# Optimization experiments

Hardware: AMD Instinct MI355X
Metric: run time of the kernel (lower is better)

## Reference

```python
import jax, jax.numpy as jnp
import numpy as np

B, T, D, H, L, F = 256, 32, 1024, 8, 3, 2048
SSRC, NCOL, NTAB, NACT, NSYM = 64, 32, 16, 64, 32
HD = D // H


def setup_inputs() -> dict:
    key = jax.random.key(0)
    ks = jax.random.split(key, 40)
    n = lambda k, s, sc=0.02: jax.random.normal(k, s, jnp.float32) * sc
    inp = {}
    inp["prev_action_emb"] = jax.random.normal(ks[0], (B, T, D), jnp.float32)
    inp["encoded_src"] = jax.random.normal(ks[1], (B, SSRC, D), jnp.float32)
    inp["encoded_col"] = jax.random.normal(ks[2], (B, NCOL, D), jnp.float32)
    inp["encoded_tab"] = jax.random.normal(ks[3], (B, NTAB, D), jnp.float32)
    inp["src_mask"] = jnp.zeros((B, SSRC), jnp.int32)  # 1 = padded
    inp["symbol_ids"] = jax.random.randint(ks[4], (B, T), 0, NSYM)
    inp["view_type"] = jax.random.randint(ks[5], (B,), 0, 3)  # 0=action,1=col,2=tab
    inp["gold_action"] = jax.random.randint(ks[6], (B,), 0, NACT)
    inp["gold_col"] = jax.random.randint(ks[7], (B,), 0, NCOL)
    inp["gold_tab"] = jax.random.randint(ks[8], (B,), 0, NTAB)
    # grammar embeddings (torch nn.Embedding default ~ N(0,1))
    inp["symbol_emb"] = jax.random.normal(ks[9], (NSYM, D), jnp.float32)
    inp["action_emb"] = jax.random.normal(ks[10], (NACT, D), jnp.float32)
    # affine heads
    inp["action_aff_w"] = n(ks[11], (D, D)); inp["action_aff_b"] = jnp.zeros((D,), jnp.float32)
    inp["symbol_aff_w"] = n(ks[12], (D, D)); inp["symbol_aff_b"] = jnp.zeros((D,), jnp.float32)
    inp["col_aff_w"] = n(ks[13], (D, D)); inp["col_aff_b"] = jnp.zeros((D,), jnp.float32)
    inp["tab_aff_w"] = n(ks[14], (D, D)); inp["tab_aff_b"] = jnp.zeros((D,), jnp.float32)
    inp["tgt_lin_w"] = n(ks[15], (2 * D, D)); inp["tgt_lin_b"] = jnp.zeros((D,), jnp.float32)
    inp["out_lin_w"] = n(ks[16], (D, D)); inp["out_lin_b"] = jnp.zeros((D,), jnp.float32)
    # transformer decoder layers (q,k,v,o stacked on axis 1)
    inp["self_w"] = n(ks[17], (L, 4, D, D)); inp["self_b"] = jnp.zeros((L, 4, D), jnp.float32)
    inp["cross_w"] = n(ks[18], (L, 4, D, D)); inp["cross_b"] = jnp.zeros((L, 4, D), jnp.float32)
    inp["ffn_w1"] = n(ks[19], (L, D, F)); inp["ffn_b1"] = jnp.zeros((L, F), jnp.float32)
    inp["ffn_w2"] = n(ks[20], (L, F, D)); inp["ffn_b2"] = jnp.zeros((L, D), jnp.float32)
    inp["ln_g"] = jnp.ones((L, 3, D), jnp.float32); inp["ln_b"] = jnp.zeros((L, 3, D), jnp.float32)
    return inp


def _pe(t, d):
    pos = jnp.arange(t, dtype=jnp.float32)[:, None]
    div = jnp.exp(jnp.arange(0, d, 2, dtype=jnp.float32) * (-np.log(10000.0) / d))
    pe = jnp.zeros((t, d), jnp.float32)
    pe = pe.at[:, 0::2].set(jnp.sin(pos * div)).at[:, 1::2].set(jnp.cos(pos * div))
    return pe


def _ln(x, g, b, eps=1e-5):
    m = jnp.mean(x, -1, keepdims=True)
    v = jnp.mean((x - m) ** 2, -1, keepdims=True)
    return (x - m) / jnp.sqrt(v + eps) * g + b


def _mha(xq, xkv, w, b, pad=None):
    # w: [4, D, D] for q,k,v,o; pad: [B, Tk] bool key-padding mask
    q = (xq @ w[0] + b[0]).reshape(xq.shape[0], -1, H, HD)
    k = (xkv @ w[1] + b[1]).reshape(xkv.shape[0], -1, H, HD)
    v = (xkv @ w[2] + b[2]).reshape(xkv.shape[0], -1, H, HD)
    s = jnp.einsum("bqhd,bkhd->bhqk", q, k) / np.sqrt(HD).astype(np.float32)
    if pad is not None:
        s = jnp.where(pad[:, None, None, :], -1e9, s)
    a = jax.nn.softmax(s, -1)
    o = jnp.einsum("bhqk,bkhd->bqhd", a, v).reshape(xq.shape[0], -1, D)
    return o @ w[3] + b[3]


def reference(prev_action_emb, encoded_src, encoded_col, encoded_tab, symbol_emb, action_emb,
              action_aff_w, action_aff_b, symbol_aff_w, symbol_aff_b, col_aff_w, col_aff_b,
              tab_aff_w, tab_aff_b, tgt_lin_w, tgt_lin_b, out_lin_w, out_lin_b,
              self_w, self_b, cross_w, cross_b, ffn_w1, ffn_b1, ffn_w2, ffn_b2, ln_g, ln_b,
              src_mask, symbol_ids, view_type, gold_action, gold_col, gold_tab):
    # target embeddings: affine(prev action emb) ++ affine(symbol emb gather)
    tgt_a = prev_action_emb @ action_aff_w + action_aff_b            # [B,T,D]
    tgt_s = symbol_emb[symbol_ids] @ symbol_aff_w + symbol_aff_b     # [B,T,D]
    x = jnp.concatenate([tgt_a, tgt_s], -1) @ tgt_lin_w + tgt_lin_b  # [B,T,D]
    x = x + _pe(T, D)[None]  # positional encoding (dropout = eval identity)
    pad = src_mask.astype(bool)
    for l in range(L):  # post-LN TransformerDecoderLayer (torch default, relu FFN)
        x = _ln(x + _mha(x, x, self_w[l], self_b[l]), ln_g[l, 0], ln_b[l, 0])
        x = _ln(x + _mha(x, encoded_src, cross_w[l], cross_b[l], pad), ln_g[l, 1], ln_b[l, 1])
        ff = jax.nn.relu(x @ ffn_w1[l] + ffn_b1[l]) @ ffn_w2[l] + ffn_b2[l]
        x = _ln(x + ff, ln_g[l, 2], ln_b[l, 2])
    out = x[:, -1, :] @ out_lin_w + out_lin_b  # [B,D], last decode position
    # three routed prediction heads: affine(src) . out -> masked log_softmax
    src_a = action_emb @ action_aff_w + action_aff_b                 # [A,D]
    logp_a = jax.nn.log_softmax(out @ src_a.T, -1)                   # [B,A]
    src_c = encoded_col @ col_aff_w + col_aff_b                      # [B,Nc,D]
    logp_c = jax.nn.log_softmax(jnp.einsum("bnd,bd->bn", src_c, out), -1)
    src_t = encoded_tab @ tab_aff_w + tab_aff_b                      # [B,Nt,D]
    logp_t = jax.nn.log_softmax(jnp.einsum("bnd,bd->bn", src_t, out), -1)
    ga = jnp.take_along_axis(logp_a, gold_action[:, None], 1)[:, 0]
    gc = jnp.take_along_axis(logp_c, gold_col[:, None], 1)[:, 0]
    gt = jnp.take_along_axis(logp_t, gold_tab[:, None], 1)[:, 0]
    # grammar routing: each example's loss comes from exactly one view
    nll = -jnp.where(view_type == 0, ga, jnp.where(view_type == 1, gc, gt))  # [B]
    return nll
```

## Files before the change

### kernel.cpp

```cpp
#include <hip/hip_runtime.h>

typedef float  f32x4 __attribute__((ext_vector_type(4)));
typedef short  s16x8 __attribute__((ext_vector_type(8)));

__device__ __forceinline__ float b2f(short s) {
    return __uint_as_float(((unsigned)(unsigned short)s) << 16);
}
__device__ __forceinline__ short f2b(float f) {
    unsigned u = __float_as_uint(f);
    u = u + 0x7fffu + ((u >> 16) & 1u);
    return (short)(u >> 16);
}

__device__ __forceinline__ void gld_lds16(const short* g, short* l) {
    __builtin_amdgcn_global_load_lds(
        (const __attribute__((address_space(1))) unsigned int*)(const void*)g,
        (__attribute__((address_space(3))) unsigned int*)(void*)l,
        16, 0, 0);
}

#define S_VMCNT0    asm volatile("s_waitcnt vmcnt(0)" ::: "memory")
#define S_LGKM0     asm volatile("s_waitcnt lgkmcnt(0)" ::: "memory")
#define SBAR        __builtin_amdgcn_s_barrier()
#define SCHED0      __builtin_amdgcn_sched_barrier(0)

template<int BM>
__global__ __launch_bounds__(512) void gemm_pipe(
    const short* __restrict__ A, const short* __restrict__ Bt,
    const float* __restrict__ bias,
    short* __restrict__ Cb,
    const short* __restrict__ res,
    const float* __restrict__ sym2, const int* __restrict__ sid,
    const float* __restrict__ pe,
    int M, int N, int K, int epi)
{
    constexpr int MF   = BM / 32;
    constexpr int ALW  = BM / 64;
    constexpr int BUFB = (BM + 256) * 128;
    __shared__ short lds[2 * (BM + 256) * 64];

    const int tid  = threadIdx.x;
    const int lane = tid & 63;
    const int wave = tid >> 6;

    int bid = blockIdx.x;
    int nwg = gridDim.x;
    if ((nwg & 7) == 0) { int q = nwg >> 3; bid = (bid & 7) * q + (bid >> 3); }
    const int nbx = N >> 8;
    const int m0 = (bid / nbx) * BM;
    const int n0 = (bid % nbx) * 256;

    const int wm = (wave >> 2) * (BM / 2);
    const int wn = (wave & 3) * 64;
    const int l15 = lane & 15, l4 = lane >> 4;
    const int key = lane & 7;

    f32x4 acc[MF][4];
#pragma unroll
    for (int m = 0; m < MF; m++)
#pragma unroll
        for (int n = 0; n < 4; n++)
#pragma unroll
            for (int j = 0; j < 4; j++) acc[m][n][j] = 0.f;

    int aoff[MF], boff[4];
#pragma unroll
    for (int m = 0; m < MF; m++) {
        int r = wm + m * 16 + l15;
        aoff[m] = r * 128 + ((l4 ^ key) << 4);
    }
#pragma unroll
    for (int n = 0; n < 4; n++) {
        int r = wn + n * 16 + l15;
        boff[n] = BM * 128 + r * 128 + ((l4 ^ key) << 4);
    }

    const int lrow = lane >> 3;
    const int lchunk = (lane & 7) ^ lrow;
    size_t agoff[ALW]; int aldo[ALW];
#pragma unroll
    for (int i = 0; i < ALW; i++) {
        int rr = wave * (BM / 8) + i * 8;
        agoff[i] = (size_t)(m0 + rr + lrow) * K + lchunk * 8;
        aldo[i]  = rr * 128;
    }
    size_t bgoff[4]; int bldo[4];
#pragma unroll
    for (int i = 0; i < 4; i++) {
        int rr = wave * 32 + i * 8;
        bgoff[i] = (size_t)(n0 + rr + lrow) * K + lchunk * 8;
        bldo[i]  = BM * 128 + rr * 128;
    }

    char* lbase = (char*)lds;
    auto stage = [&](int kt, int bufoff) {
        char* lb = lbase + bufoff;
        const size_t ke = (size_t)kt * 64;
#pragma unroll
        for (int i = 0; i < ALW; i++)
            gld_lds16(A + agoff[i] + ke, (short*)(lb + aldo[i]));
#pragma unroll
        for (int i = 0; i < 4; i++)
            gld_lds16(Bt + bgoff[i] + ke, (short*)(lb + bldo[i]));
    };

    const int NT = K >> 6;
    stage(0, 0);
    S_VMCNT0; SCHED0; SBAR; SCHED0;

    int cb = 0;
    for (int t = 0; t < NT; t++) {
        if (t + 1 < NT) stage(t + 1, (cb ^ 1) * BUFB);
        const char* cp = lbase + cb * BUFB;
        {
            s16x8 af[MF], bv[4];
#pragma unroll
            for (int m = 0; m < MF; m++) af[m] = *(const s16x8*)(cp + aoff[m]);
#pragma unroll
            for (int n = 0; n < 4; n++)  bv[n] = *(const s16x8*)(cp + boff[n]);
            S_LGKM0; SCHED0;
            __builtin_amdgcn_s_setprio(1);
#pragma unroll
            for (int m = 0; m < MF; m++)
#pragma unroll
                for (int n = 0; n < 4; n++)
                    acc[m][n] = __builtin_amdgcn_mfma_f32_16x16x32_bf16(
                        af[m], bv[n], acc[m][n], 0, 0, 0);
            __builtin_amdgcn_s_setprio(0);
        }
        {
            s16x8 af[MF], bv[4];
#pragma unroll
            for (int m = 0; m < MF; m++) af[m] = *(const s16x8*)(cp + (aoff[m] ^ 64));
#pragma unroll
            for (int n = 0; n < 4; n++)  bv[n] = *(const s16x8*)(cp + (boff[n] ^ 64));
            S_LGKM0; SCHED0;
            __builtin_amdgcn_s_setprio(1);
#pragma unroll
            for (int m = 0; m < MF; m++)
#pragma unroll
                for (int n = 0; n < 4; n++)
                    acc[m][n] = __builtin_amdgcn_mfma_f32_16x16x32_bf16(
                        af[m], bv[n], acc[m][n], 0, 0, 0);
            __builtin_amdgcn_s_setprio(0);
        }
        S_VMCNT0; SCHED0; SBAR; SCHED0;
        cb ^= 1;
    }

#pragma unroll
    for (int m = 0; m < MF; m++) {
#pragma unroll
        for (int n = 0; n < 4; n++) {
#pragma unroll
            for (int j = 0; j < 4; j++) {
                int row = m0 + wm + m * 16 + l4 * 4 + j;
                int col = n0 + wn + n * 16 + l15;
                float v = acc[m][n][j];
                if (bias) v += bias[col];
                size_t idx = (size_t)row * N + col;
                if (epi == 0) {
                    Cb[idx] = f2b(v);
                } else if (epi == 2) {
                    v += sym2[(size_t)sid[row] * 1024 + col] + pe[(size_t)(row & 31) * 1024 + col];
                    Cb[idx] = f2b(v);
                } else if (epi == 3) {
                    Cb[idx] = f2b(fmaxf(v, 0.f));
                } else {
                    Cb[idx] = f2b(v + b2f(res[idx]));
                }
            }
        }
    }
}

__global__ __launch_bounds__(256) void gemm_bt(
    const short* __restrict__ A, const short* __restrict__ Bt,
    const float* __restrict__ bias,
    float* __restrict__ Cf, short* __restrict__ Cb,
    const short* __restrict__ res,
    int M, int N, int K, int epi)
{
    __shared__ short As[128 * 64];
    __shared__ short Bs[128 * 64];
    const int tid  = threadIdx.x;
    const int lane = tid & 63;
    const int wave = tid >> 6;
    const int m0 = blockIdx.y * 128, n0 = blockIdx.x * 128;
    const int wm = (wave >> 1) * 64, wn = (wave & 1) * 64;
    const int l15 = lane & 15, l4 = lane >> 4;

    f32x4 acc[4][4];
#pragma unroll
    for (int m = 0; m < 4; m++)
#pragma unroll
        for (int n = 0; n < 4; n++)
#pragma unroll
            for (int j = 0; j < 4; j++) acc[m][n][j] = 0.f;

    const int srow = wave * 32 + (lane >> 3);
    const int scol = (lane & 7) * 8;
    const short* Ag = A  + (size_t)(m0 + srow) * K + scol;
    const short* Bg = Bt + (size_t)(n0 + srow) * K + scol;
    short* Al = As + (wave * 32) * 64;
    short* Bl = Bs + (wave * 32) * 64;

    for (int k0 = 0; k0 < K; k0 += 64) {
#pragma unroll
        for (int i = 0; i < 4; i++) {
            gld_lds16(Ag + (size_t)(i * 8) * K + k0, Al + i * 8 * 64);
            gld_lds16(Bg + (size_t)(i * 8) * K + k0, Bl + i * 8 * 64);
        }
        __syncthreads();
#pragma unroll
        for (int kk = 0; kk < 64; kk += 32) {
            s16x8 af[4], bfv[4];
#pragma unroll
            for (int m = 0; m < 4; m++)
                af[m] = *(const s16x8*)(As + (wm + m * 16 + l15) * 64 + kk + l4 * 8);
#pragma unroll
            for (int n = 0; n < 4; n++)
                bfv[n] = *(const s16x8*)(Bs + (wn + n * 16 + l15) * 64 + kk + l4 * 8);
#pragma unroll
            for (int m = 0; m < 4; m++)
#pragma unroll
                for (int n = 0; n < 4; n++)
                    acc[m][n] = __builtin_amdgcn_mfma_f32_16x16x32_bf16(
                        af[m], bfv[n], acc[m][n], 0, 0, 0);
        }
        __syncthreads();
    }

#pragma unroll
    for (int m = 0; m < 4; m++) {
#pragma unroll
        for (int n = 0; n < 4; n++) {
#pragma unroll
            for (int j = 0; j < 4; j++) {
                int row = m0 + wm + m * 16 + l4 * 4 + j;
                int col = n0 + wn + n * 16 + l15;
                float v = acc[m][n][j];
                if (bias) v += bias[col];
                size_t idx = (size_t)row * N + col;
                if (epi == 0) {
                    Cb[idx] = f2b(v);
                } else if (epi == 1) {
                    Cf[idx] = v;
                } else if (epi == 3) {
                    Cb[idx] = f2b(fmaxf(v, 0.f));
                } else if (epi == 6) {
                    Cb[idx] = f2b(v + b2f(res[idx]));
                } else {
                    Cf[idx] = v; Cb[idx] = f2b(v);
                }
            }
        }
    }
}

__global__ __launch_bounds__(256) void attn_self(const short* __restrict__ qkv,
                                                 short* __restrict__ o)
{
    const int b = blockIdx.x >> 3, h = blockIdx.x & 7;
    __shared__ short Q[32 * 128], Kk[32 * 128], Vv[32 * 128];
    __shared__ float S[32 * 32];
    const int tid = threadIdx.x;
    const size_t base = (size_t)b * 32 * 3072 + h * 128;
    for (int i = tid; i < 512; i += 256) {
        int r = i >> 4, c = (i & 15) * 8;
        size_t g = base + (size_t)r * 3072 + c;
        *(s16x8*)(Q  + r * 128 + c) = *(const s16x8*)(qkv + g);
        *(s16x8*)(Kk + r * 128 + c) = *(const s16x8*)(qkv + g + 1024);
        *(s16x8*)(Vv + r * 128 + c) = *(const s16x8*)(qkv + g + 2048);
    }
    __syncthreads();
    for (int i = tid; i < 1024; i += 256) {
        int r = i >> 5, c = i & 31;
        float s = 0.f;
        for (int d8 = 0; d8 < 16; d8++) {
            s16x8 qa = *(const s16x8*)(Q  + r * 128 + d8 * 8);
            s16x8 ka = *(const s16x8*)(Kk + c * 128 + d8 * 8);
#pragma unroll
            for (int j = 0; j < 8; j++) s += b2f(qa[j]) * b2f(ka[j]);
        }
        S[i] = s * 0.088388347648318447f;
    }
    __syncthreads();
    if (tid < 32) {
        float mx = -1e30f;
        for (int c = 0; c < 32; c++) mx = fmaxf(mx, S[tid * 32 + c]);
        float sum = 0.f;
        for (int c = 0; c < 32; c++) { float p = __expf(S[tid * 32 + c] - mx); S[tid * 32 + c] = p; sum += p; }
        float inv = 1.f / sum;
        for (int c = 0; c < 32; c++) S[tid * 32 + c] *= inv;
    }
    __syncthreads();
    for (int i = tid; i < 4096; i += 256) {
        int r = i >> 7, d = i & 127;
        float a = 0.f;
        for (int c = 0; c < 32; c++) a += S[r * 32 + c] * b2f(Vv[c * 128 + d]);
        o[(size_t)(b * 32 + r) * 1024 + h * 128 + d] = f2b(a);
    }
}

__global__ __launch_bounds__(256) void attn_cross(const short* __restrict__ q_,
                                                  const short* __restrict__ ckv,
                                                  const int* __restrict__ mask,
                                                  short* __restrict__ o)
{
    const int b = blockIdx.x >> 3, h = blockIdx.x & 7;
    __shared__ short Q[32 * 128], Kk[64 * 128], Vv[64 * 128];
    __shared__ float S[32 * 64];
    const int tid = threadIdx.x;
    for (int i = tid; i < 512; i += 256) {
        int r = i >> 4, c = (i & 15) * 8;
        *(s16x8*)(Q + r * 128 + c) = *(const s16x8*)(q_ + (size_t)(b * 32 + r) * 1024 + h * 128 + c);
    }
    for (int i = tid; i < 1024; i += 256) {
        int r = i >> 4, c = (i & 15) * 8;
        size_t g = (size_t)(b * 64 + r) * 2048 + h * 128 + c;
        *(s16x8*)(Kk + r * 128 + c) = *(const s16x8*)(ckv + g);
        *(s16x8*)(Vv + r * 128 + c) = *(const s16x8*)(ckv + g + 1024);
    }
    __syncthreads();
    for (int i = tid; i < 2048; i += 256) {
        int r = i >> 6, c = i & 63;
        float s = 0.f;
        for (int d8 = 0; d8 < 16; d8++) {
            s16x8 qa = *(const s16x8*)(Q  + r * 128 + d8 * 8);
            s16x8 ka = *(const s16x8*)(Kk + c * 128 + d8 * 8);
#pragma unroll
            for (int j = 0; j < 8; j++) s += b2f(qa[j]) * b2f(ka[j]);
        }
        s *= 0.088388347648318447f;
        if (mask[b * 64 + c] != 0) s = -1e9f;
        S[i] = s;
    }
    __syncthreads();
    if (tid < 32) {
        float mx = -1e30f;
        for (int c = 0; c < 64; c++) mx = fmaxf(mx, S[tid * 64 + c]);
        float sum = 0.f;
        for (int c = 0; c < 64; c++) { float p = __expf(S[tid * 64 + c] - mx); S[tid * 64 + c] = p; sum += p; }
        float inv = 1.f / sum;
        for (int c = 0; c < 64; c++) S[tid * 64 + c] *= inv;
    }
    __syncthreads();
    for (int i = tid; i < 4096; i += 256) {
        int r = i >> 7, d = i & 127;
        float a = 0.f;
        for (int c = 0; c < 64; c++) a += S[r * 64 + c] * b2f(Vv[c * 128 + d]);
        o[(size_t)(b * 32 + r) * 1024 + h * 128 + d] = f2b(a);
    }
}

__global__ __launch_bounds__(256) void attn_self_last(const short* __restrict__ q,
                                                      const short* __restrict__ kv,
                                                      short* __restrict__ out)
{
    __shared__ float qs[4][128];
    __shared__ float ps[4][32];
    const int wave = threadIdx.x >> 6, lane = threadIdx.x & 63;
    const int idx = blockIdx.x * 4 + wave;
    const int b = idx >> 3, h = idx & 7;
    for (int d = lane; d < 128; d += 64)
        qs[wave][d] = b2f(q[(size_t)b * 1024 + h * 128 + d]);
    __syncthreads();
    float s = -1e30f;
    if (lane < 32) {
        const short* kr = kv + (size_t)(b * 32 + lane) * 2048 + h * 128;
        float a = 0.f;
        for (int d = 0; d < 128; d += 8) {
            s16x8 kvv = *(const s16x8*)(kr + d);
#pragma unroll
            for (int j = 0; j < 8; j++) a += qs[wave][d + j] * b2f(kvv[j]);
        }
        s = a * 0.088388347648318447f;
    }
    float mx = s;
#pragma unroll
    for (int o = 1; o < 32; o <<= 1) mx = fmaxf(mx, __shfl_xor(mx, o));
    float p = (lane < 32) ? __expf(s - mx) : 0.f;
    float sum = p;
#pragma unroll
    for (int o = 1; o < 32; o <<= 1) sum += __shfl_xor(sum, o);
    if (lane < 32) ps[wave][lane] = p / sum;
    __syncthreads();
    for (int d = lane; d < 128; d += 64) {
        float a = 0.f;
        for (int j = 0; j < 32; j++)
            a += ps[wave][j] * b2f(kv[(size_t)(b * 32 + j) * 2048 + 1024 + h * 128 + d]);
        out[(size_t)b * 1024 + h * 128 + d] = f2b(a);
    }
}

__global__ __launch_bounds__(256) void attn_cross_last(const short* __restrict__ q,
                                                       const short* __restrict__ ckv,
                                                       const int* __restrict__ mask,
                                                       short* __restrict__ out)
{
    __shared__ float qs[4][128];
    __shared__ float ps[4][64];
    const int wave = threadIdx.x >> 6, lane = threadIdx.x & 63;
    const int idx = blockIdx.x * 4 + wave;
    const int b = idx >> 3, h = idx & 7;
    for (int d = lane; d < 128; d += 64)
        qs[wave][d] = b2f(q[(size_t)b * 1024 + h * 128 + d]);
    __syncthreads();
    const short* kr = ckv + (size_t)(b * 64 + lane) * 2048 + h * 128;
    float a = 0.f;
    for (int d = 0; d < 128; d += 8) {
        s16x8 kvv = *(const s16x8*)(kr + d);
#pragma unroll
        for (int j = 0; j < 8; j++) a += qs[wave][d + j] * b2f(kvv[j]);
    }
    float s = a * 0.088388347648318447f;
    if (mask[b * 64 + lane] != 0) s = -1e9f;
    float mx = s;
#pragma unroll
    for (int o = 1; o < 64; o <<= 1) mx = fmaxf(mx, __shfl_xor(mx, o));
    float p = __expf(s - mx);
    float sum = p;
#pragma unroll
    for (int o = 1; o < 64; o <<= 1) sum += __shfl_xor(sum, o);
    ps[wave][lane] = p / sum;
    __syncthreads();
    for (int d = lane; d < 128; d += 64) {
        float acc = 0.f;
        for (int j = 0; j < 64; j++)
            acc += ps[wave][j] * b2f(ckv[(size_t)(b * 64 + j) * 2048 + 1024 + h * 128 + d]);
        out[(size_t)b * 1024 + h * 128 + d] = f2b(acc);
    }
}

__global__ __launch_bounds__(128) void ln_rows_b(const short* __restrict__ X,
                                                 short* __restrict__ Y,
                                                 const float* __restrict__ g,
                                                 const float* __restrict__ bt)
{
    const int row = blockIdx.x, tid = threadIdx.x;
    s16x8 v = *(const s16x8*)(X + (size_t)row * 1024 + tid * 8);
    float f[8];
    float s = 0.f, q = 0.f;
#pragma unroll
    for (int j = 0; j < 8; j++) { f[j] = b2f(v[j]); s += f[j]; q += f[j] * f[j]; }
#pragma unroll
    for (int o = 1; o < 64; o <<= 1) { s += __shfl_xor(s, o); q += __shfl_xor(q, o); }
    __shared__ float ls[2], lq[2];
    if ((tid & 63) == 0) { ls[tid >> 6] = s; lq[tid >> 6] = q; }
    __syncthreads();
    s = ls[0] + ls[1];
    q = lq[0] + lq[1];
    const float mean = s * 0.0009765625f;
    const float var  = q * 0.0009765625f - mean * mean;
    const float rs = rsqrtf(var + 1e-5f);
    s16x8 ov;
#pragma unroll
    for (int j = 0; j < 8; j++) {
        int c = tid * 8 + j;
        ov[j] = f2b((f[j] - mean) * rs * g[c] + bt[c]);
    }
    *(s16x8*)(Y + (size_t)row * 1024 + tid * 8) = ov;
}

__global__ __launch_bounds__(256) void convf2b(const float* __restrict__ s,
                                               short* __restrict__ d, int n)
{
    int i = (blockIdx.x * 256 + threadIdx.x) * 8;
    if (i < n) {
        float4 a = *(const float4*)(s + i);
        float4 b = *(const float4*)(s + i + 4);
        s16x8 o;
        o[0] = f2b(a.x); o[1] = f2b(a.y); o[2] = f2b(a.z); o[3] = f2b(a.w);
        o[4] = f2b(b.x); o[5] = f2b(b.y); o[6] = f2b(b.z); o[7] = f2b(b.w);
        *(s16x8*)(d + i) = o;
    }
}

__global__ __launch_bounds__(256) void transpose_conv_b(const float* __restrict__ src0,
                                                        short* __restrict__ dst0,
                                                        int R, int C)
{
    const float* src = src0 + (size_t)blockIdx.z * R * C;
    short* dst = dst0 + (size_t)blockIdx.z * R * C;
    __shared__ float t[32][33];
    int c0 = blockIdx.x * 32, r0 = blockIdx.y * 32;
    int tx = threadIdx.x & 31, ty = threadIdx.x >> 5;
#pragma unroll
    for (int i = 0; i < 32; i += 8) t[ty + i][tx] = src[(size_t)(r0 + ty + i) * C + c0 + tx];
    __syncthreads();
#pragma unroll
    for (int i = 0; i < 32; i += 8) dst[(size_t)(c0 + ty + i) * R + r0 + tx] = f2b(t[tx][ty + i]);
}

__global__ __launch_bounds__(256) void pad_conv(const float* __restrict__ s,
                                                short* __restrict__ d, int src_rows)
{
    int i = blockIdx.x * 256 + threadIdx.x;
    int r = i >> 10;
    d[i] = (r < src_rows) ? f2b(s[i]) : (short)0;
}

__global__ __launch_bounds__(256) void pe_build(float* __restrict__ pe)
{
    int i = blockIdx.x * 256 + threadIdx.x;
    int t = i >> 10, d = i & 1023;
    int de = d & ~1;
    float ang = (float)t * expf((float)de * (-9.2103403719761836f / 1024.f));
    pe[i] = (d & 1) ? cosf(ang) : sinf(ang);
}

__global__ __launch_bounds__(256) void gather_last(const short* __restrict__ x,
                                                   short* __restrict__ xlast)
{
    int i = blockIdx.x * 256 + threadIdx.x;
    int b = i >> 10, d = i & 1023;
    xlast[i] = x[((size_t)(b * 32 + 31) << 10) + d];
}

__global__ __launch_bounds__(64) void head_final(
    const float* __restrict__ logits_a,
    const float* __restrict__ enc_col_f, const short* __restrict__ yc,
    const float* __restrict__ enc_tab_f, const short* __restrict__ yt,
    const float* __restrict__ outf,
    const float* __restrict__ col_b, const float* __restrict__ tab_b,
    const int* __restrict__ view, const int* __restrict__ ga,
    const int* __restrict__ gc, const int* __restrict__ gt,
    float* __restrict__ nll)
{
    const int b = blockIdx.x, lane = threadIdx.x;
    const int vt = view[b];
    if (vt == 0) {
        float x = logits_a[(size_t)b * 128 + lane];
        float mx = x;
#pragma unroll
        for (int o = 1; o < 64; o <<= 1) mx = fmaxf(mx, __shfl_xor(mx, o));
        float sum = __expf(x - mx);
#pragma unroll
        for (int o = 1; o < 64; o <<= 1) sum += __shfl_xor(sum, o);
        float lse = mx + logf(sum);
        float gl = __shfl(x, ga[b]);
        if (lane == 0) nll[b] = lse - gl;
    } else {
        const int nit = (vt == 1) ? 32 : 16;
        const float* enc = (vt == 1) ? (enc_col_f + (size_t)b * 32 * 1024)
                                     : (enc_tab_f + (size_t)b * 16 * 1024);
        const short* y   = (vt == 1) ? (yc + (size_t)b * 1024) : (yt + (size_t)b * 1024);
        const float* bb  = (vt == 1) ? col_b : tab_b;
        float bc = 0.f;
        for (int i = lane; i < 1024; i += 64) bc += bb[i] * outf[(size_t)b * 1024 + i];
#pragma unroll
        for (int o = 1; o < 64; o <<= 1) bc += __shfl_xor(bc, o);
        float logit = -1e30f;
        if (lane < nit) {
            float s = bc;
            const float* er = enc + (size_t)lane * 1024;
            for (int d8 = 0; d8 < 128; d8++) {
                s16x8 yv = *(const s16x8*)(y + d8 * 8);
                float4 e0 = *(const float4*)(er + d8 * 8);
                float4 e1 = *(const float4*)(er + d8 * 8 + 4);
                s += e0.x * b2f(yv[0]) + e0.y * b2f(yv[1]) + e0.z * b2f(yv[2]) + e0.w * b2f(yv[3])
                   + e1.x * b2f(yv[4]) + e1.y * b2f(yv[5]) + e1.z * b2f(yv[6]) + e1.w * b2f(yv[7]);
            }
            logit = s;
        }
        float mx = logit;
#pragma unroll
        for (int o = 1; o < 64; o <<= 1) mx = fmaxf(mx, __shfl_xor(mx, o));
        float sum = (lane < nit) ? __expf(logit - mx) : 0.f;
#pragma unroll
        for (int o = 1; o < 64; o <<= 1) sum += __shfl_xor(sum, o);
        float lse = mx + logf(sum);
        int g = (vt == 1) ? gc[b] : gt[b];
        float gl = __shfl(logit, g);
        if (lane == 0) nll[b] = lse - gl;
    }
}

extern "C" void kernel_launch(void* const* d_in, const int* in_sizes, int n_in,
                              void* d_out, int out_size, void* d_ws, size_t ws_size,
                              hipStream_t stream)
{
    const float* pa_f     = (const float*)d_in[0];
    const float* src_f    = (const float*)d_in[1];
    const float* colenc_f = (const float*)d_in[2];
    const float* tabenc_f = (const float*)d_in[3];
    const int*   src_mask = (const int*)d_in[4];
    const int*   sym_ids  = (const int*)d_in[5];
    const int*   view     = (const int*)d_in[6];
    const int*   gold_a   = (const int*)d_in[7];
    const int*   gold_c   = (const int*)d_in[8];
    const int*   gold_t   = (const int*)d_in[9];
    const float* sym_emb  = (const float*)d_in[10];
    const float* act_emb  = (const float*)d_in[11];
    const float* Aaff_w   = (const float*)d_in[12];
    const float* Aaff_b   = (const float*)d_in[13];
    const float* Saff_w   = (const float*)d_in[14];
    const float* Saff_b   = (const float*)d_in[15];
    const float* Caff_w   = (const float*)d_in[16];
    const float* Caff_b   = (const float*)d_in[17];
    const float* Taff_w   = (const float*)d_in[18];
    const float* Taff_b   = (const float*)d_in[19];
    const float* tgt_w    = (const float*)d_in[20];
    const float* tgt_b    = (const float*)d_in[21];
    const float* outw     = (const float*)d_in[22];
    const float* outbias  = (const float*)d_in[23];
    const float* self_w   = (const float*)d_in[24];
    const float* self_b   = (const float*)d_in[25];
    const float* cross_w  = (const float*)d_in[26];
    const float* cross_b  = (const float*)d_in[27];
    const float* f1w      = (const float*)d_in[28];
    const float* f1b      = (const float*)d_in[29];
    const float* f2w      = (const float*)d_in[30];
    const float* f2bb     = (const float*)d_in[31];
    const float* lng      = (const float*)d_in[32];
    const float* lnbt     = (const float*)d_in[33];
    float* nll = (float*)d_out;

    char* ws = (char*)d_ws;
    size_t off = 0;
    auto alloc = [&](size_t bytes) -> char* {
        off = (off + 255) & ~(size_t)255;
        char* p = ws + off; off += bytes; return p;
    };

    const size_t MB1 = (size_t)1024 * 1024;
    short* WAaff  = (short*)alloc(MB1 * 2);
    short* WSaff  = (short*)alloc(MB1 * 2);
    short* Wtop   = (short*)alloc(MB1 * 2);
    short* Wbot   = (short*)alloc(MB1 * 2);
    short* Wout   = (short*)alloc(MB1 * 2);
    short* Wcol   = (short*)alloc(MB1 * 2);
    short* Wtab   = (short*)alloc(MB1 * 2);
    short* Wself  = (short*)alloc(12 * MB1 * 2);
    short* Wcross = (short*)alloc(12 * MB1 * 2);
    short* Wf1a   = (short*)alloc(3 * 2 * MB1 * 2);
    short* Wf2a   = (short*)alloc(3 * 2 * MB1 * 2);

    short* src_bf   = (short*)alloc((size_t)16384 * 1024 * 2);
    short* sym_pad  = (short*)alloc((size_t)128 * 1024 * 2);
    short* act_pad  = (short*)alloc((size_t)128 * 1024 * 2);
    short* sa_out   = (short*)alloc((size_t)128 * 1024 * 2);
    float* sym2     = (float*)alloc((size_t)128 * 1024 * 4);
    float* pe       = (float*)alloc((size_t)32 * 1024 * 4);
    short* tgt_a    = (short*)alloc((size_t)8192 * 1024 * 2);
    short* x_bf     = (short*)alloc((size_t)8192 * 1024 * 2);
    short* tmpb     = (short*)alloc((size_t)8192 * 1024 * 2);
    short* arena    = (short*)alloc((size_t)16384 * 2048 * 2);
    short* xlast    = (short*)alloc((size_t)256 * 1024 * 2);
    float* outf     = (float*)alloc((size_t)256 * 1024 * 4);
    short* outb16   = (short*)alloc((size_t)256 * 1024 * 2);
    short* srca     = (short*)alloc((size_t)128 * 1024 * 2);
    float* logits_a = (float*)alloc((size_t)256 * 128 * 4);
    short* ycb      = (short*)alloc((size_t)256 * 1024 * 2);
    short* ytb      = (short*)alloc((size_t)256 * 1024 * 2);
    short* xq31     = (short*)alloc((size_t)256 * 1024 * 2);
    short* x256a    = (short*)alloc((size_t)256 * 1024 * 2);
    short* x256b    = (short*)alloc((size_t)256 * 1024 * 2);
    short* q256     = (short*)alloc((size_t)256 * 1024 * 2);
    short* cq256    = (short*)alloc((size_t)256 * 1024 * 2);
    short* o256     = (short*)alloc((size_t)256 * 1024 * 2);
    short* h256     = (short*)alloc((size_t)256 * 2048 * 2);
    short* tmpb256  = (short*)alloc((size_t)256 * 1024 * 2);

    short* pa_bf = tmpb;
    short* cq    = tmpb;
    short* attn  = tgt_a;

    const dim3 BLK(256);
    auto conv = [&](const float* s, short* d, size_t n) {
        convf2b<<<dim3((unsigned)(n / 8 / 256)), BLK, 0, stream>>>(s, d, (int)n);
    };
    auto trans = [&](const float* s, short* d, int R, int C, int nm) {
        transpose_conv_b<<<dim3(C / 32, R / 32, nm), BLK, 0, stream>>>(s, d, R, C);
    };
    auto gp = [&](const short* A, const short* Bt, const float* bias,
                  short* Cb, const short* res,
                  const float* sy, const int* si, const float* pp,
                  int M, int N, int K, int epi, int BM) {
        if (BM == 256)
            gemm_pipe<256><<<dim3((N / 256) * (M / 256)), dim3(512), 0, stream>>>(
                A, Bt, bias, Cb, res, sy, si, pp, M, N, K, epi);
        else
            gemm_pipe<128><<<dim3((N / 256) * (M / 128)), dim3(512), 0, stream>>>(
                A, Bt, bias, Cb, res, sy, si, pp, M, N, K, epi);
    };
    auto gsm = [&](const short* A, const short* Bt, const float* bias,
                   float* Cf, short* Cb, const short* res,
                   int M, int N, int K, int epi) {
        gemm_bt<<<dim3(N / 128, M / 128), BLK, 0, stream>>>(
            A, Bt, bias, Cf, Cb, res, M, N, K, epi);
    };

    pe_build<<<dim3(128), BLK, 0, stream>>>(pe);
    conv(pa_f, pa_bf, (size_t)8192 * 1024);
    conv(src_f, src_bf, (size_t)16384 * 1024);
    conv(Caff_w, Wcol, MB1);
    conv(Taff_w, Wtab, MB1);
    pad_conv<<<dim3(512), BLK, 0, stream>>>(sym_emb, sym_pad, 32);
    pad_conv<<<dim3(512), BLK, 0, stream>>>(act_emb, act_pad, 64);
    trans(Aaff_w, WAaff, 1024, 1024, 1);
    trans(Saff_w, WSaff, 1024, 1024, 1);
    trans(tgt_w, Wtop, 1024, 1024, 1);
    trans(tgt_w + MB1, Wbot, 1024, 1024, 1);
    trans(outw, Wout, 1024, 1024, 1);
    trans(self_w, Wself, 1024, 1024, 12);
    trans(cross_w, Wcross, 1024, 1024, 12);
    trans(f1w, Wf1a, 1024, 2048, 3);
    trans(f2w, Wf2a, 2048, 1024, 3);

    gsm(sym_pad, WSaff, Saff_b, nullptr, sa_out, nullptr, 128, 1024, 1024, 0);
    gsm(sa_out, Wbot, nullptr, sym2, nullptr, nullptr, 128, 1024, 1024, 1);
    gp(pa_bf, WAaff, Aaff_b, tgt_a, nullptr, nullptr, nullptr, nullptr,
       8192, 1024, 1024, 0, 128);
    gp(tgt_a, Wtop, tgt_b, x_bf, nullptr, sym2, sym_ids, pe,
       8192, 1024, 1024, 2, 128);

    for (int l = 0; l < 2; l++) {
        const float* sb = self_b + (size_t)l * 4096;
        const float* cb = cross_b + (size_t)l * 4096;
        gp(x_bf, Wself + (size_t)(4 * l) * MB1, sb, arena, nullptr, nullptr, nullptr, nullptr,
           8192, 3072, 1024, 0, 256);
        attn_self<<<dim3(2048), BLK, 0, stream>>>(arena, attn);
        gp(attn, Wself + (size_t)(4 * l + 3) * MB1, sb + 3072, tmpb, x_bf, nullptr, nullptr, nullptr,
           8192, 1024, 1024, 6, 128);
        ln_rows_b<<<dim3(8192), dim3(128), 0, stream>>>(tmpb, x_bf,
            lng + (size_t)(l * 3 + 0) * 1024, lnbt + (size_t)(l * 3 + 0) * 1024);
        gp(x_bf, Wcross + (size_t)(4 * l) * MB1, cb, cq, nullptr, nullptr, nullptr, nullptr,
           8192, 1024, 1024, 0, 128);
        gp(src_bf, Wcross + (size_t)(4 * l + 1) * MB1, cb + 1024, arena, nullptr, nullptr, nullptr, nullptr,
           16384, 2048, 1024, 0, 256);
        attn_cross<<<dim3(2048), BLK, 0, stream>>>(cq, arena, src_mask, attn);
        gp(attn, Wcross + (size_t)(4 * l + 3) * MB1, cb + 3072, tmpb, x_bf, nullptr, nullptr, nullptr,
           8192, 1024, 1024, 6, 128);
        ln_rows_b<<<dim3(8192), dim3(128), 0, stream>>>(tmpb, x_bf,
            lng + (size_t)(l * 3 + 1) * 1024, lnbt + (size_t)(l * 3 + 1) * 1024);
        gp(x_bf, Wf1a + (size_t)l * 2 * MB1, f1b + (size_t)l * 2048, arena, nullptr, nullptr, nullptr, nullptr,
           8192, 2048, 1024, 3, 256);
        gp(arena, Wf2a + (size_t)l * 2 * MB1, f2bb + (size_t)l * 1024, tmpb, x_bf, nullptr, nullptr, nullptr,
           8192, 1024, 2048, 6, 128);
        ln_rows_b<<<dim3(8192), dim3(128), 0, stream>>>(tmpb, x_bf,
            lng + (size_t)(l * 3 + 2) * 1024, lnbt + (size_t)(l * 3 + 2) * 1024);
    }

    {
        const float* sb = self_b + (size_t)2 * 4096;
        const float* cb = cross_b + (size_t)2 * 4096;
        gather_last<<<dim3(1024), BLK, 0, stream>>>(x_bf, xq31);
        gp(x_bf, Wself + (size_t)(4 * 2 + 1) * MB1, sb + 1024, arena, nullptr, nullptr, nullptr, nullptr,
           8192, 2048, 1024, 0, 256);
        gsm(xq31, Wself + (size_t)(4 * 2) * MB1, sb, nullptr, q256, nullptr, 256, 1024, 1024, 0);
        attn_self_last<<<dim3(512), BLK, 0, stream>>>(q256, arena, o256);
        gsm(o256, Wself + (size_t)(4 * 2 + 3) * MB1, sb + 3072, nullptr, tmpb256, xq31, 256, 1024, 1024, 6);
        ln_rows_b<<<dim3(256), dim3(128), 0, stream>>>(tmpb256, x256a,
            lng + (size_t)(2 * 3 + 0) * 1024, lnbt + (size_t)(2 * 3 + 0) * 1024);
        gsm(x256a, Wcross + (size_t)(4 * 2) * MB1, cb, nullptr, cq256, nullptr, 256, 1024, 1024, 0);
        gp(src_bf, Wcross + (size_t)(4 * 2 + 1) * MB1, cb + 1024, arena, nullptr, nullptr, nullptr, nullptr,
           16384, 2048, 1024, 0, 256);
        attn_cross_last<<<dim3(512), BLK, 0, stream>>>(cq256, arena, src_mask, o256);
        gsm(o256, Wcross + (size_t)(4 * 2 + 3) * MB1, cb + 3072, nullptr, tmpb256, x256a, 256, 1024, 1024, 6);
        ln_rows_b<<<dim3(256), dim3(128), 0, stream>>>(tmpb256, x256b,
            lng + (size_t)(2 * 3 + 1) * 1024, lnbt + (size_t)(2 * 3 + 1) * 1024);
        gsm(x256b, Wf1a + (size_t)2 * 2 * MB1, f1b + (size_t)2 * 2048, nullptr, h256, nullptr,
            256, 2048, 1024, 3);
        gsm(h256, Wf2a + (size_t)2 * 2 * MB1, f2bb + (size_t)2 * 1024, nullptr, tmpb256, x256b,
            256, 1024, 2048, 6);
        ln_rows_b<<<dim3(256), dim3(128), 0, stream>>>(tmpb256, xlast,
            lng + (size_t)(2 * 3 + 2) * 1024, lnbt + (size_t)(2 * 3 + 2) * 1024);
    }

    gsm(xlast, Wout, outbias, outf, outb16, nullptr, 256, 1024, 1024, 5);
    gsm(act_pad, WAaff, Aaff_b, nullptr, srca, nullptr, 128, 1024, 1024, 0);
    gsm(outb16, srca, nullptr, logits_a, nullptr, nullptr, 256, 128, 1024, 1);
    gsm(outb16, Wcol, nullptr, nullptr, ycb, nullptr, 256, 1024, 1024, 0);
    gsm(outb16, Wtab, nullptr, nullptr, ytb, nullptr, 256, 1024, 1024, 0);
    head_final<<<dim3(256), dim3(64), 0, stream>>>(
        logits_a, colenc_f, ycb, tabenc_f, ytb, outf,
        Caff_b, Taff_b, view, gold_a, gold_c, gold_t, nll);
}
```

Baseline: 2.521 ms.

## Fold action affine into target linear weight and vectorize attention PV

Precomputes a combined weight (Wtop·Aaff) and combined bias so the two chained 8192x1024x1024 GEMMs on prev_action_emb collapse into one, removing a full large GEMM and its intermediate buffer. The combined weight is computed once per call with a small 1024^3 GEMM plus a vector-matrix bias kernel. Separately, the self and cross attention kernels now do softmax with float4 LDS accesses, and each thread of the PV product accumulates 8 output columns using vectorized V loads and 16-byte stores. The weight folding adds an extra bf16 rounding of the combined weight, which slightly changes numerics.

```diff
diff --git a/kernel.cpp b/kernel.cpp
--- a/kernel.cpp
+++ b/kernel.cpp
@@ -258,6 +258,17 @@
     }
 }
 
+__global__ __launch_bounds__(256) void vecmat_bias(const float* __restrict__ Ab,
+                                                   const float* __restrict__ Wt,
+                                                   const float* __restrict__ tb,
+                                                   float* __restrict__ out)
+{
+    int j = blockIdx.x * 256 + threadIdx.x;
+    float s = tb[j];
+    for (int k = 0; k < 1024; k++) s += Ab[k] * Wt[(size_t)k * 1024 + j];
+    out[j] = s;
+}
+
 __global__ __launch_bounds__(256) void attn_self(const short* __restrict__ qkv,
                                                  short* __restrict__ o)
 {
@@ -287,19 +298,44 @@
     }
     __syncthreads();
     if (tid < 32) {
+        float4* row = (float4*)(S + tid * 32);
         float mx = -1e30f;
-        for (int c = 0; c < 32; c++) mx = fmaxf(mx, S[tid * 32 + c]);
+#pragma unroll
+        for (int c = 0; c < 8; c++) {
+            float4 v4 = row[c];
+            mx = fmaxf(mx, fmaxf(fmaxf(v4.x, v4.y), fmaxf(v4.z, v4.w)));
+        }
         float sum = 0.f;
-        for (int c = 0; c < 32; c++) { float p = __expf(S[tid * 32 + c] - mx); S[tid * 32 + c] = p; sum += p; }
+#pragma unroll
+        for (int c = 0; c < 8; c++) {
+            float4 v4 = row[c];
+            v4.x = __expf(v4.x - mx); v4.y = __expf(v4.y - mx);
+            v4.z = __expf(v4.z - mx); v4.w = __expf(v4.w - mx);
+            sum += v4.x + v4.y + v4.z + v4.w;
+            row[c] = v4;
+        }
         float inv = 1.f / sum;
-        for (int c = 0; c < 32; c++) S[tid * 32 + c] *= inv;
-    }
-    __syncthreads();
-    for (int i = tid; i < 4096; i += 256) {
-        int r = i >> 7, d = i & 127;
-        float a = 0.f;
-        for (int c = 0; c < 32; c++) a += S[r * 32 + c] * b2f(Vv[c * 128 + d]);
-        o[(size_t)(b * 32 + r) * 1024 + h * 128 + d] = f2b(a);
+#pragma unroll
+        for (int c = 0; c < 8; c++) {
+            float4 v4 = row[c];
+            v4.x *= inv; v4.y *= inv; v4.z *= inv; v4.w *= inv;
+            row[c] = v4;
+        }
+    }
+    __syncthreads();
+    for (int g = tid; g < 512; g += 256) {
+        int r = g >> 4, d0 = (g & 15) * 8;
+        float a8[8] = {0.f,0.f,0.f,0.f,0.f,0.f,0.f,0.f};
+        for (int c = 0; c < 32; c++) {
+            float p = S[r * 32 + c];
+            s16x8 v = *(const s16x8*)(Vv + c * 128 + d0);
+#pragma unroll
+            for (int j = 0; j < 8; j++) a8[j] += p * b2f(v[j]);
+        }
+        s16x8 ov;
+#pragma unroll
+        for (int j = 0; j < 8; j++) ov[j] = f2b(a8[j]);
+        *(s16x8*)(o + (size_t)(b * 32 + r) * 1024 + h * 128 + d0) = ov;
     }
 }
 
@@ -338,19 +374,44 @@
     }
     __syncthreads();
     if (tid < 32) {
+        float4* row = (float4*)(S + tid * 64);
         float mx = -1e30f;
-        for (int c = 0; c < 64; c++) mx = fmaxf(mx, S[tid * 64 + c]);
+#pragma unroll
+        for (int c = 0; c < 16; c++) {
+            float4 v4 = row[c];
+            mx = fmaxf(mx, fmaxf(fmaxf(v4.x, v4.y), fmaxf(v4.z, v4.w)));
+        }
         float sum = 0.f;
-        for (int c = 0; c < 64; c++) { float p = __expf(S[tid * 64 + c] - mx); S[tid * 64 + c] = p; sum += p; }
+#pragma unroll
+        for (int c = 0; c < 16; c++) {
+            float4 v4 = row[c];
+            v4.x = __expf(v4.x - mx); v4.y = __expf(v4.y - mx);
+            v4.z = __expf(v4.z - mx); v4.w = __expf(v4.w - mx);
+            sum += v4.x + v4.y + v4.z + v4.w;
+            row[c] = v4;
+        }
         float inv = 1.f / sum;
-        for (int c = 0; c < 64; c++) S[tid * 64 + c] *= inv;
-    }
-    __syncthreads();
-    for (int i = tid; i < 4096; i += 256) {
-        int r = i >> 7, d = i & 127;
-        float a = 0.f;
-        for (int c = 0; c < 64; c++) a += S[r * 64 + c] * b2f(Vv[c * 128 + d]);
-        o[(size_t)(b * 32 + r) * 1024 + h * 128 + d] = f2b(a);
+#pragma unroll
+        for (int c = 0; c < 16; c++) {
+            float4 v4 = row[c];
+            v4.x *= inv; v4.y *= inv; v4.z *= inv; v4.w *= inv;
+            row[c] = v4;
+        }
+    }
+    __syncthreads();
+    for (int g = tid; g < 512; g += 256) {
+        int r = g >> 4, d0 = (g & 15) * 8;
+        float a8[8] = {0.f,0.f,0.f,0.f,0.f,0.f,0.f,0.f};
+        for (int c = 0; c < 64; c++) {
+            float p = S[r * 64 + c];
+            s16x8 v = *(const s16x8*)(Vv + c * 128 + d0);
+#pragma unroll
+            for (int j = 0; j < 8; j++) a8[j] += p * b2f(v[j]);
+        }
+        s16x8 ov;
+#pragma unroll
+        for (int j = 0; j < 8; j++) ov[j] = f2b(a8[j]);
+        *(s16x8*)(o + (size_t)(b * 32 + r) * 1024 + h * 128 + d0) = ov;
     }
 }
 
@@ -632,6 +693,9 @@
     short* Wout   = (short*)alloc(MB1 * 2);
     short* Wcol   = (short*)alloc(MB1 * 2);
     short* Wtab   = (short*)alloc(MB1 * 2);
+    short* Aaffrm = (short*)alloc(MB1 * 2);
+    short* Wcomb  = (short*)alloc(MB1 * 2);
+    float* cbias  = (float*)alloc(1024 * 4);
     short* Wself  = (short*)alloc(12 * MB1 * 2);
     short* Wcross = (short*)alloc(12 * MB1 * 2);
     short* Wf1a   = (short*)alloc(3 * 2 * MB1 * 2);
@@ -643,7 +707,7 @@
     short* sa_out   = (short*)alloc((size_t)128 * 1024 * 2);
     float* sym2     = (float*)alloc((size_t)128 * 1024 * 4);
     float* pe       = (float*)alloc((size_t)32 * 1024 * 4);
-    short* tgt_a    = (short*)alloc((size_t)8192 * 1024 * 2);
+    short* attn     = (short*)alloc((size_t)8192 * 1024 * 2);
     short* x_bf     = (short*)alloc((size_t)8192 * 1024 * 2);
     short* tmpb     = (short*)alloc((size_t)8192 * 1024 * 2);
     short* arena    = (short*)alloc((size_t)16384 * 2048 * 2);
@@ -665,7 +729,6 @@
 
     short* pa_bf = tmpb;
     short* cq    = tmpb;
-    short* attn  = tgt_a;
 
     const dim3 BLK(256);
     auto conv = [&](const float* s, short* d, size_t n) {
@@ -697,6 +760,7 @@
     conv(src_f, src_bf, (size_t)16384 * 1024);
     conv(Caff_w, Wcol, MB1);
     conv(Taff_w, Wtab, MB1);
+    conv(Aaff_w, Aaffrm, MB1);
     pad_conv<<<dim3(512), BLK, 0, stream>>>(sym_emb, sym_pad, 32);
     pad_conv<<<dim3(512), BLK, 0, stream>>>(act_emb, act_pad, 64);
     trans(Aaff_w, WAaff, 1024, 1024, 1);
@@ -709,11 +773,11 @@
     trans(f1w, Wf1a, 1024, 2048, 3);
     trans(f2w, Wf2a, 2048, 1024, 3);
 
+    gsm(Wtop, Aaffrm, nullptr, nullptr, Wcomb, nullptr, 1024, 1024, 1024, 0);
+    vecmat_bias<<<dim3(4), BLK, 0, stream>>>(Aaff_b, tgt_w, tgt_b, cbias);
     gsm(sym_pad, WSaff, Saff_b, nullptr, sa_out, nullptr, 128, 1024, 1024, 0);
     gsm(sa_out, Wbot, nullptr, sym2, nullptr, nullptr, 128, 1024, 1024, 1);
-    gp(pa_bf, WAaff, Aaff_b, tgt_a, nullptr, nullptr, nullptr, nullptr,
-       8192, 1024, 1024, 0, 128);
-    gp(tgt_a, Wtop, tgt_b, x_bf, nullptr, sym2, sym_ids, pe,
+    gp(pa_bf, Wcomb, cbias, x_bf, nullptr, sym2, sym_ids, pe,
        8192, 1024, 1024, 2, 128);
 
     for (int l = 0; l < 2; l++) {
```

Measured after the change: 2.535 ms. About the same (+0.5%).
